# Performance work log

Hardware: AMD Instinct MI355X
Metric: run time of the kernel (lower is better)

The kernel has to match this reference:

```python
import jax, jax.numpy as jnp
import numpy as np

Q_SHAPE = 256      # query block length (default query_shape=(256,))
FLANGE = 256       # memory flange (default memory_flange=(256,))
MAX_REL = 513      # default max_relative_position


def setup_inputs() -> dict:
    key = jax.random.key(0)
    ks = jax.random.split(key, 5)
    B, H, L, D = 2, 8, 8192, 64
    q = jax.random.normal(ks[0], (B, H, L, D), jnp.float32)
    k = jax.random.normal(ks[1], (B, H, L, D), jnp.float32)
    v = jax.random.normal(ks[2], (B, H, L, D), jnp.float32)
    vocab = 2 * MAX_REL + 1
    rel_k_emb = jax.random.normal(ks[3], (vocab, D), jnp.float32) * 0.02
    rel_v_emb = jax.random.normal(ks[4], (vocab, D), jnp.float32) * 0.02
    return {"q": q, "k": k, "v": v, "rel_k_emb": rel_k_emb, "rel_v_emb": rel_v_emb}


def _rel_positions(len_q, len_k, max_rel):
    # generate_relative_positions_matrix: queries aligned to the END of the
    # memory block (range_vec_q = range_vec_k[-len_q:]).
    rk = jnp.arange(len_k)
    rq = rk[-len_q:]
    dist = rk[None, :] - rq[:, None]            # [len_q, len_k]
    return jnp.clip(dist, -max_rel, max_rel) + max_rel


def _masked_local_attention(q, k, v, rel_k_emb, rel_v_emb):
    B, H, L, D = q.shape
    qs, f = Q_SHAPE, FLANGE
    nb = L // qs                                 # number of query blocks
    nf = f // qs
    hp = jax.lax.Precision.HIGHEST

    # fold heads into batch; scale queries.
    qb = (q * (D ** -0.5)).reshape(B * H, nb, qs, D)

    # masked memory blocks: pad LEFT by flange, then memory block i is the
    # concat of blocks [i, ..., i+nf] of the padded sequence -> width qs+f.
    kp = jnp.pad(k.reshape(B * H, L, D), ((0, 0), (f, 0), (0, 0))).reshape(B * H, nb + nf, qs, D)
    vp = jnp.pad(v.reshape(B * H, L, D), ((0, 0), (f, 0), (0, 0))).reshape(B * H, nb + nf, qs, D)
    km = jnp.concatenate([kp[:, s:s + nb] for s in range(nf + 1)], axis=-2)  # [BH, nb, qs+f, D]
    vm = jnp.concatenate([vp[:, s:s + nb] for s in range(nf + 1)], axis=-2)

    mlen = qs + f
    rel = _rel_positions(qs, mlen, MAX_REL)      # [qs, qs+f]
    rk = rel_k_emb[rel]                          # [qs, qs+f, D]
    rv = rel_v_emb[rel]

    # relative_attention_inner (transpose=True): content + position logits.
    logits = (jnp.einsum('bnxd,bnyd->bnxy', qb, km, precision=hp)
              + jnp.einsum('bnxd,xyd->bnxy', qb, rk, precision=hp))

    # causal local mask: global_mem = n*qs - f + mi must satisfy
    # 0 <= global_mem <= global_query = n*qs + qi.
    n = jnp.arange(nb)[:, None, None]
    qi = jnp.arange(qs)[None, :, None]
    mi = jnp.arange(mlen)[None, None, :]
    valid = (mi - f <= qi) & (n * qs + mi >= f)  # [nb, qs, qs+f]
    logits = jnp.where(valid[None], logits, -1e9)

    w = jax.nn.softmax(logits, axis=-1)

    # relative_attention_inner (transpose=False): values + relative values.
    out = (jnp.einsum('bnxy,bnyd->bnxd', w, vm, precision=hp)
           + jnp.einsum('bnxy,xyd->bnxd', w, rv, precision=hp))
    return out.reshape(B, H, L, D)


def reference(q, k, v, rel_k_emb, rel_v_emb):
    return _masked_local_attention(q, k, v, rel_k_emb, rel_v_emb)
```

## Files before the change

kernel.cpp:

```cpp
#include <hip/hip_runtime.h>

typedef __bf16 bf16x8 __attribute__((ext_vector_type(8)));
typedef __bf16 bf16x4 __attribute__((ext_vector_type(4)));
typedef float f32x4 __attribute__((ext_vector_type(4)));

#define LSEQ 8192
#define DDIM 64
#define QS 256
#define CHUNK 128
#define VOCAB 1027
#define RELK_ELEMS (VOCAB * DDIM)
#define RELVT_PITCH 768
#define RELVT_ELEMS (DDIM * RELVT_PITCH)
#define SMAX 10.0f
#define QSCALE 0.18033688011112042f

#define WS_RELK_OFF 0
#define WS_RELVT_OFF 131456
#define WS_KIMG_OFF 229888
#define WS_VIMG_OFF (WS_KIMG_OFF + 16777216)
#define WS_NEED ((size_t)WS_VIMG_OFF + 16777216)

__device__ __forceinline__ int swze(int row) { return ((row ^ (row >> 3)) & 7) << 3; }

__device__ __forceinline__ f32x4 mfma16(bf16x8 a, bf16x8 b, f32x4 c) {
  return __builtin_amdgcn_mfma_f32_16x16x32_bf16(a, b, c, 0, 0, 0);
}

__device__ __forceinline__ float fexp2(float x) { return __builtin_exp2f(x); }

__device__ __forceinline__ void gload16(const __bf16* g, __bf16* l) {
  __builtin_amdgcn_global_load_lds(
      (const __attribute__((address_space(1))) void*)g,
      (__attribute__((address_space(3))) void*)l, 16, 0, 0);
}

__device__ __forceinline__ bf16x8 cvt8(float4 a, float4 b, float sc) {
  bf16x8 r;
  r[0] = (__bf16)(a.x * sc); r[1] = (__bf16)(a.y * sc);
  r[2] = (__bf16)(a.z * sc); r[3] = (__bf16)(a.w * sc);
  r[4] = (__bf16)(b.x * sc); r[5] = (__bf16)(b.y * sc);
  r[6] = (__bf16)(b.z * sc); r[7] = (__bf16)(b.w * sc);
  return r;
}

__global__ void prep_rel(const float* __restrict__ rk, const float* __restrict__ rv,
                         __bf16* __restrict__ relk, __bf16* __restrict__ relvT) {
  int i = blockIdx.x * 256 + threadIdx.x;
  if (i < RELK_ELEMS) relk[i] = (__bf16)rk[i];
  if (i < RELVT_ELEMS) {
    int d = i / RELVT_PITCH, j = i - d * RELVT_PITCH;
    relvT[i] = (__bf16)rv[(j + 2) * DDIM + d];
  }
}

__global__ void prep_kimg(const float* __restrict__ k, __bf16* __restrict__ kimg) {
  int i = blockIdx.x * 256 + threadIdx.x;
  int b = i & 1023;
  int bt = i >> 10;
  int y = b >> 3;
  int d0 = ((b & 7) * 8) ^ swze(y);
  const float* src = k + ((size_t)bt * 128 + y) * DDIM + d0;
  float4 a = *(const float4*)src;
  float4 bb = *(const float4*)(src + 4);
  *(bf16x8*)(kimg + (size_t)i * 8) = cvt8(a, bb, 1.0f);
}

__global__ void prep_vimg(const float* __restrict__ v, __bf16* __restrict__ vimg) {
  __shared__ __align__(16) __bf16 t[CHUNK * DDIM];
  const int bt = blockIdx.x;
  const int tid = threadIdx.x;
  const float* vb = v + (size_t)bt * CHUNK * DDIM;
#pragma unroll
  for (int rep = 0; rep < 4; ++rep) {
    int e = (rep * 256 + tid) * 8;
    float4 a = *(const float4*)(vb + e);
    float4 b = *(const float4*)(vb + e + 4);
    *(bf16x8*)&t[e] = cvt8(a, b, 1.0f);
  }
  __syncthreads();
#pragma unroll
  for (int rep = 0; rep < 4; ++rep) {
    int b = rep * 256 + tid;
    int d = b >> 4;
    int y0 = ((b & 15) * 8) ^ swze(d);
    bf16x8 o8;
#pragma unroll
    for (int j = 0; j < 8; ++j) o8[j] = t[(y0 + j) * DDIM + d];
    *(bf16x8*)(vimg + (size_t)bt * 8192 + (size_t)b * 8) = o8;
  }
}

template <bool PRECONV>
__global__ __launch_bounds__(256, 2) void attn_kernel(
    const float* __restrict__ qg, const float* __restrict__ kg, const float* __restrict__ vg,
    const __bf16* __restrict__ relk, const __bf16* __restrict__ relvT,
    const __bf16* __restrict__ kimg, const __bf16* __restrict__ vimg,
    float* __restrict__ outg) {
  __shared__ __align__(16) __bf16 kbuf[CHUNK * DDIM];
  __shared__ __align__(16) __bf16 vbuf[CHUNK * DDIM];
  __shared__ __align__(16) __bf16 pbuf[64 * CHUNK];
  __shared__ __bf16 ring[4][2][16][18];

  const int phys = blockIdx.x;
  const int xcd = phys & 7;
  const int mseq = phys >> 3;
  const int rg = mseq & 3;
  const int gl = mseq >> 2;
  const int pair = xcd * 64 + gl;
  const int bh = pair >> 5;
  const int nblk = pair & 31;

  const int tid = threadIdx.x;
  const int w = tid >> 6;
  const int lane = tid & 63;
  const int c16 = lane & 15;
  const int grp = lane >> 4;

  const int row_base = rg * 64 + 16 * w;
  const int c0w = 194 - row_base;
  const int j0w = 192 - row_base;
  const int prow = 16 * w + c16;

  const int cstart = (nblk == 0) ? 2 : 0;
  const int c_hi = (rg >= 2) ? 4 : 3;

  auto stage_k = [&](int c) {
    if constexpr (PRECONV) {
      const __bf16* base = kimg + (((size_t)bh * 64 + (size_t)(2 * nblk - 2 + c)) << 13);
      const int boff = 256 * w;
#pragma unroll
      for (int rep = 0; rep < 4; ++rep)
        gload16(base + (size_t)(boff + 64 * rep + lane) * 8, &kbuf[(boff + 64 * rep) * 8]);
    } else {
      const int ty = tid >> 3, td = tid & 7, d0 = td * 8;
      const float* kb = kg + ((size_t)bh * LSEQ + (size_t)(2 * nblk - 2 + c) * CHUNK) * DDIM;
#pragma unroll
      for (int rep = 0; rep < 4; ++rep) {
        int yc = ty + rep * 32;
        const float4* sp = (const float4*)(kb + yc * DDIM + d0);
        *(bf16x8*)&kbuf[yc * 64 + (d0 ^ swze(yc))] = cvt8(sp[0], sp[1], 1.0f);
      }
    }
  };
  auto stage_v = [&](int c) {
    if constexpr (PRECONV) {
      const __bf16* base = vimg + (((size_t)bh * 64 + (size_t)(2 * nblk - 2 + c)) << 13);
      const int boff = 256 * w;
#pragma unroll
      for (int rep = 0; rep < 4; ++rep)
        gload16(base + (size_t)(boff + 64 * rep + lane) * 8, &vbuf[(boff + 64 * rep) * 8]);
    } else {
      const int ty = tid >> 3, td = tid & 7, d0 = td * 8;
      const float* vb = vg + ((size_t)bh * LSEQ + (size_t)(2 * nblk - 2 + c) * CHUNK) * DDIM;
#pragma unroll
      for (int rep = 0; rep < 4; ++rep) {
        int yc = ty + rep * 32;
        const float4* sp = (const float4*)(vb + yc * DDIM + d0);
        float ff[8] = {sp[0].x, sp[0].y, sp[0].z, sp[0].w, sp[1].x, sp[1].y, sp[1].z, sp[1].w};
#pragma unroll
        for (int i = 0; i < 8; ++i) {
          int d = d0 + i;
          vbuf[d * CHUNK + (yc ^ swze(d))] = (__bf16)ff[i];
        }
      }
    }
  };

  bf16x8 qa[2];
  {
    const float* qrow = qg + (size_t)(bh * LSEQ + nblk * QS + row_base + c16) * DDIM;
#pragma unroll
    for (int kk = 0; kk < 2; ++kk) {
      const float4* sp = (const float4*)(qrow + kk * 32 + grp * 8);
      qa[kk] = cvt8(sp[0], sp[1], QSCALE);
    }
  }

  f32x4 o[4];
#pragma unroll
  for (int jd = 0; jd < 4; ++jd) o[jd] = f32x4{0.f, 0.f, 0.f, 0.f};
  float lsum = 0.f;

  auto qr_tile = [&](int ju) {
    f32x4 acc = {0.f, 0.f, 0.f, 0.f};
    int t = c0w + 16 * ju + c16;
    const bf16x8* b0 = (const bf16x8*)(relk + t * DDIM + 8 * grp);
    const bf16x8* b1 = (const bf16x8*)(relk + t * DDIM + 32 + 8 * grp);
    acc = mfma16(*b0, qa[0], acc);
    acc = mfma16(*b1, qa[1], acc);
#pragma unroll
    for (int r = 0; r < 4; ++r) ring[w][ju & 1][4 * grp + r][c16] = (__bf16)acc[r];
  };

  stage_k(cstart);
  __syncthreads();

  for (int c = cstart; c < c_hi; ++c) {
    const bool active = (4 * rg + w + 17 - 8 * c) > 0;

    stage_v(c);

    if (active) {
      if (c == cstart) qr_tile(8 * c + 3);
      float ps = 0.f;
#pragma unroll
      for (int jtl = 0; jtl < 8; ++jtl) {
        const int jt = 8 * c + jtl;
        qr_tile(jt + 4);
        f32x4 acc = {-SMAX, -SMAX, -SMAX, -SMAX};
        int krow = 16 * jtl + c16;
        const bf16x8 aK0 = *(const bf16x8*)&kbuf[krow * 64 + ((8 * grp) ^ swze(krow))];
        const bf16x8 aK1 = *(const bf16x8*)&kbuf[krow * 64 + ((32 + 8 * grp) ^ swze(krow))];
        acc = mfma16(aK0, qa[0], acc);
        acc = mfma16(aK1, qa[1], acc);
        bf16x4 pw;
#pragma unroll
        for (int r = 0; r < 4; ++r) {
          int sk = 4 * grp + r + 15 - c16;
          float qrv = (float)ring[w][(jt + 3 + (sk >> 4)) & 1][sk & 15][c16];
          int yv = 16 * jt + 4 * grp + r;
          float arg = (yv <= row_base + c16 + 256) ? (acc[r] + qrv) : -1e9f;
          float pv = fexp2(arg);
          ps += pv;
          pw[r] = (__bf16)pv;
        }
        *(bf16x4*)&pbuf[prow * CHUNK + ((16 * jtl + 4 * grp) ^ swze(prow))] = pw;
      }
      lsum += ps;
    }

    __syncthreads();

    if (c + 1 < c_hi) stage_k(c + 1);

    if (active) {
      __builtin_amdgcn_s_setprio(1);
#pragma unroll
      for (int ks = 0; ks < 4; ++ks) {
        bf16x8 aP = *(const bf16x8*)&pbuf[prow * CHUNK + ((32 * ks + 8 * grp) ^ swze(prow))];
#pragma unroll
        for (int jd = 0; jd < 4; ++jd) {
          int drow = 16 * jd + c16;
          bf16x8 bV = *(const bf16x8*)&vbuf[drow * CHUNK + ((32 * ks + 8 * grp) ^ swze(drow))];
          o[jd] = mfma16(aP, bV, o[jd]);
        }
      }
      __builtin_amdgcn_s_setprio(0);
#pragma unroll
      for (int s2 = 0; s2 < 5; ++s2) {
        bf16x8 aW;
#pragma unroll
        for (int i = 0; i < 8; ++i) {
          int yl = 32 * s2 + 8 * grp + i + c16 - 31;
          __bf16 pv = (__bf16)0.f;
          if (yl >= 0 && yl < CHUNK) pv = pbuf[prow * CHUNK + (yl ^ swze(prow))];
          aW[i] = pv;
        }
        const int u0 = 128 * c + 32 + 32 * s2 + 8 * grp;
#pragma unroll
        for (int jd = 0; jd < 4; ++jd) {
          int d = 16 * jd + c16;
          const bf16x8* bR = (const bf16x8*)(relvT + d * RELVT_PITCH + j0w + u0);
          o[jd] = mfma16(aW, *bR, o[jd]);
        }
      }
    }

    __syncthreads();
  }

  lsum += __shfl_xor(lsum, 16);
  lsum += __shfl_xor(lsum, 32);
  float inv = 1.0f / lsum;
  float* ob = outg + (size_t)(bh * LSEQ + nblk * QS + row_base) * DDIM;
#pragma unroll
  for (int r = 0; r < 4; ++r) {
    float ir = __shfl(inv, 4 * grp + r);
#pragma unroll
    for (int jd = 0; jd < 4; ++jd) {
      ob[(4 * grp + r) * DDIM + 16 * jd + c16] = o[jd][r] * ir;
    }
  }
}

extern "C" void kernel_launch(void* const* d_in, const int* in_sizes, int n_in,
                              void* d_out, int out_size, void* d_ws, size_t ws_size,
                              hipStream_t stream) {
  const float* q = (const float*)d_in[0];
  const float* k = (const float*)d_in[1];
  const float* v = (const float*)d_in[2];
  const float* rk = (const float*)d_in[3];
  const float* rv = (const float*)d_in[4];

  char* ws = (char*)d_ws;
  __bf16* relk = (__bf16*)(ws + WS_RELK_OFF);
  __bf16* relvT = (__bf16*)(ws + WS_RELVT_OFF);
  __bf16* kimg = (__bf16*)(ws + WS_KIMG_OFF);
  __bf16* vimg = (__bf16*)(ws + WS_VIMG_OFF);

  prep_rel<<<257, 256, 0, stream>>>(rk, rv, relk, relvT);
  if (ws_size >= WS_NEED) {
    prep_kimg<<<4096, 256, 0, stream>>>(k, kimg);
    prep_vimg<<<1024, 256, 0, stream>>>(v, vimg);
    attn_kernel<true><<<2048, 256, 0, stream>>>(q, k, v, relk, relvT, kimg, vimg, (float*)d_out);
  } else {
    attn_kernel<false><<<2048, 256, 0, stream>>>(q, k, v, relk, relvT, relk, relk, (float*)d_out);
  }
}
```

Before: 188.5 us.

## Process two 64-row query groups per block to share staged K/V tiles

Each workgroup now handles two query row groups (rows p*64 and p*64+128) instead of one, halving the grid and reusing each staged K and V chunk across both groups. This removes duplicated global-to-LDS staging of K/V chunks across blocks and balances causal work by pairing a light and a heavy row group. In exchange, register pressure doubles for accumulators and Q fragments, LDS use grows for the doubled pbuf and ring, and occupancy may drop at launch bounds of 2 blocks per CU.

Result: slower. 331.3 us (+75.7%).

```diff
diff --git a/kernel.cpp b/kernel.cpp
--- a/kernel.cpp
+++ b/kernel.cpp
@@ -99,14 +99,14 @@
     float* __restrict__ outg) {
   __shared__ __align__(16) __bf16 kbuf[CHUNK * DDIM];
   __shared__ __align__(16) __bf16 vbuf[CHUNK * DDIM];
-  __shared__ __align__(16) __bf16 pbuf[64 * CHUNK];
-  __shared__ __bf16 ring[4][2][16][18];
+  __shared__ __align__(16) __bf16 pbuf[2 * 64 * CHUNK];
+  __shared__ __bf16 ring[2 * 4 * 2 * 16 * 18];
 
   const int phys = blockIdx.x;
   const int xcd = phys & 7;
   const int mseq = phys >> 3;
-  const int rg = mseq & 3;
-  const int gl = mseq >> 2;
+  const int p = mseq & 1;
+  const int gl = mseq >> 1;
   const int pair = xcd * 64 + gl;
   const int bh = pair >> 5;
   const int nblk = pair & 31;
@@ -117,13 +117,21 @@
   const int c16 = lane & 15;
   const int grp = lane >> 4;
 
-  const int row_base = rg * 64 + 16 * w;
-  const int c0w = 194 - row_base;
-  const int j0w = 192 - row_base;
+  const int row_baseA = 64 * p + 16 * w;
+  const int row_baseB = row_baseA + 128;
+  const int c0wA = 194 - row_baseA;
+  const int c0wB = c0wA - 128;
+  const int j0wA = 192 - row_baseA;
+  const int j0wB = j0wA - 128;
   const int prow = 16 * w + c16;
+  const int xA16 = 4 * p + w;
+
+  __bf16* ringA = &ring[(0 * 4 + w) * 576];
+  __bf16* ringB = &ring[(1 * 4 + w) * 576];
+  __bf16* pbufA = &pbuf[0];
+  __bf16* pbufB = &pbuf[64 * CHUNK];
 
   const int cstart = (nblk == 0) ? 2 : 0;
-  const int c_hi = (rg >= 2) ? 4 : 3;
 
   auto stage_k = [&](int c) {
     if constexpr (PRECONV) {
@@ -167,102 +175,128 @@
     }
   };
 
-  bf16x8 qa[2];
+  bf16x8 qaA[2], qaB[2];
   {
-    const float* qrow = qg + (size_t)(bh * LSEQ + nblk * QS + row_base + c16) * DDIM;
+    const float* qrA = qg + (size_t)(bh * LSEQ + nblk * QS + row_baseA + c16) * DDIM;
+    const float* qrB = qg + (size_t)(bh * LSEQ + nblk * QS + row_baseB + c16) * DDIM;
 #pragma unroll
     for (int kk = 0; kk < 2; ++kk) {
-      const float4* sp = (const float4*)(qrow + kk * 32 + grp * 8);
-      qa[kk] = cvt8(sp[0], sp[1], QSCALE);
-    }
-  }
-
-  f32x4 o[4];
-#pragma unroll
-  for (int jd = 0; jd < 4; ++jd) o[jd] = f32x4{0.f, 0.f, 0.f, 0.f};
-  float lsum = 0.f;
-
-  auto qr_tile = [&](int ju) {
+      const float4* sA = (const float4*)(qrA + kk * 32 + grp * 8);
+      const float4* sB = (const float4*)(qrB + kk * 32 + grp * 8);
+      qaA[kk] = cvt8(sA[0], sA[1], QSCALE);
+      qaB[kk] = cvt8(sB[0], sB[1], QSCALE);
+    }
+  }
+
+  f32x4 oA[4], oB[4];
+#pragma unroll
+  for (int jd = 0; jd < 4; ++jd) { oA[jd] = f32x4{0.f,0.f,0.f,0.f}; oB[jd] = f32x4{0.f,0.f,0.f,0.f}; }
+  float lsumA = 0.f, lsumB = 0.f;
+
+  auto qr_tile = [&](int ju, int c0w_, __bf16* ring_, const bf16x8* qa_) {
     f32x4 acc = {0.f, 0.f, 0.f, 0.f};
-    int t = c0w + 16 * ju + c16;
+    int t = c0w_ + 16 * ju + c16;
     const bf16x8* b0 = (const bf16x8*)(relk + t * DDIM + 8 * grp);
     const bf16x8* b1 = (const bf16x8*)(relk + t * DDIM + 32 + 8 * grp);
-    acc = mfma16(*b0, qa[0], acc);
-    acc = mfma16(*b1, qa[1], acc);
-#pragma unroll
-    for (int r = 0; r < 4; ++r) ring[w][ju & 1][4 * grp + r][c16] = (__bf16)acc[r];
+    acc = mfma16(*b0, qa_[0], acc);
+    acc = mfma16(*b1, qa_[1], acc);
+#pragma unroll
+    for (int r = 0; r < 4; ++r) ring_[(ju & 1) * 288 + (4 * grp + r) * 18 + c16] = (__bf16)acc[r];
+  };
+
+  auto gstep = [&](int jt, bf16x8 aK0, bf16x8 aK1, int c0w_, int row_base_,
+                   __bf16* ring_, __bf16* pbuf_, const bf16x8* qa_, int jtl) -> float {
+    qr_tile(jt + 4, c0w_, ring_, qa_);
+    f32x4 acc = {-SMAX, -SMAX, -SMAX, -SMAX};
+    acc = mfma16(aK0, qa_[0], acc);
+    acc = mfma16(aK1, qa_[1], acc);
+    bf16x4 pw;
+    float ps = 0.f;
+#pragma unroll
+    for (int r = 0; r < 4; ++r) {
+      int sk = 4 * grp + r + 15 - c16;
+      float qrv = (float)ring_[(((jt + 3 + (sk >> 4)) & 1)) * 288 + (sk & 15) * 18 + c16];
+      int yv = 16 * jt + 4 * grp + r;
+      float arg = (yv <= row_base_ + c16 + 256) ? (acc[r] + qrv) : -1e9f;
+      float pv = fexp2(arg);
+      ps += pv;
+      pw[r] = (__bf16)pv;
+    }
+    *(bf16x4*)&pbuf_[prow * CHUNK + ((16 * jtl + 4 * grp) ^ swze(prow))] = pw;
+    return ps;
   };
 
   stage_k(cstart);
   __syncthreads();
 
-  for (int c = cstart; c < c_hi; ++c) {
-    const bool active = (4 * rg + w + 17 - 8 * c) > 0;
+  for (int c = cstart; c < 4; ++c) {
+    const bool activeA = (xA16 + 17 - 8 * c) > 0;
 
     stage_v(c);
 
-    if (active) {
-      if (c == cstart) qr_tile(8 * c + 3);
-      float ps = 0.f;
+    {
+      if (c == cstart) {
+        if (activeA) qr_tile(8 * c + 3, c0wA, ringA, qaA);
+        qr_tile(8 * c + 3, c0wB, ringB, qaB);
+      }
+      float psA = 0.f, psB = 0.f;
 #pragma unroll
       for (int jtl = 0; jtl < 8; ++jtl) {
         const int jt = 8 * c + jtl;
-        qr_tile(jt + 4);
-        f32x4 acc = {-SMAX, -SMAX, -SMAX, -SMAX};
-        int krow = 16 * jtl + c16;
+        const int krow = 16 * jtl + c16;
         const bf16x8 aK0 = *(const bf16x8*)&kbuf[krow * 64 + ((8 * grp) ^ swze(krow))];
         const bf16x8 aK1 = *(const bf16x8*)&kbuf[krow * 64 + ((32 + 8 * grp) ^ swze(krow))];
-        acc = mfma16(aK0, qa[0], acc);
-        acc = mfma16(aK1, qa[1], acc);
-        bf16x4 pw;
-#pragma unroll
-        for (int r = 0; r < 4; ++r) {
-          int sk = 4 * grp + r + 15 - c16;
-          float qrv = (float)ring[w][(jt + 3 + (sk >> 4)) & 1][sk & 15][c16];
-          int yv = 16 * jt + 4 * grp + r;
-          float arg = (yv <= row_base + c16 + 256) ? (acc[r] + qrv) : -1e9f;
-          float pv = fexp2(arg);
-          ps += pv;
-          pw[r] = (__bf16)pv;
+        if (activeA) psA += gstep(jt, aK0, aK1, c0wA, row_baseA, ringA, pbufA, qaA, jtl);
+        psB += gstep(jt, aK0, aK1, c0wB, row_baseB, ringB, pbufB, qaB, jtl);
+      }
+      lsumA += psA;
+      lsumB += psB;
+    }
+
+    __syncthreads();
+
+    if (c + 1 < 4) stage_k(c + 1);
+
+    {
+      __builtin_amdgcn_s_setprio(1);
+#pragma unroll
+      for (int ks = 0; ks < 4; ++ks) {
+        const int po = ((32 * ks + 8 * grp) ^ swze(prow));
+        bf16x8 aPA, aPB;
+        if (activeA) aPA = *(const bf16x8*)&pbufA[prow * CHUNK + po];
+        aPB = *(const bf16x8*)&pbufB[prow * CHUNK + po];
+#pragma unroll
+        for (int jd = 0; jd < 4; ++jd) {
+          const int drow = 16 * jd + c16;
+          const bf16x8 bV = *(const bf16x8*)&vbuf[drow * CHUNK + ((32 * ks + 8 * grp) ^ swze(drow))];
+          if (activeA) oA[jd] = mfma16(aPA, bV, oA[jd]);
+          oB[jd] = mfma16(aPB, bV, oB[jd]);
         }
-        *(bf16x4*)&pbuf[prow * CHUNK + ((16 * jtl + 4 * grp) ^ swze(prow))] = pw;
-      }
-      lsum += ps;
-    }
-
-    __syncthreads();
-
-    if (c + 1 < c_hi) stage_k(c + 1);
-
-    if (active) {
-      __builtin_amdgcn_s_setprio(1);
-#pragma unroll
-      for (int ks = 0; ks < 4; ++ks) {
-        bf16x8 aP = *(const bf16x8*)&pbuf[prow * CHUNK + ((32 * ks + 8 * grp) ^ swze(prow))];
-#pragma unroll
-        for (int jd = 0; jd < 4; ++jd) {
-          int drow = 16 * jd + c16;
-          bf16x8 bV = *(const bf16x8*)&vbuf[drow * CHUNK + ((32 * ks + 8 * grp) ^ swze(drow))];
-          o[jd] = mfma16(aP, bV, o[jd]);
-        }
       }
       __builtin_amdgcn_s_setprio(0);
 #pragma unroll
       for (int s2 = 0; s2 < 5; ++s2) {
-        bf16x8 aW;
+        bf16x8 aWA, aWB;
 #pragma unroll
         for (int i = 0; i < 8; ++i) {
           int yl = 32 * s2 + 8 * grp + i + c16 - 31;
-          __bf16 pv = (__bf16)0.f;
-          if (yl >= 0 && yl < CHUNK) pv = pbuf[prow * CHUNK + (yl ^ swze(prow))];
-          aW[i] = pv;
+          __bf16 pA = (__bf16)0.f, pB = (__bf16)0.f;
+          if (yl >= 0 && yl < CHUNK) {
+            int off = prow * CHUNK + (yl ^ swze(prow));
+            if (activeA) pA = pbufA[off];
+            pB = pbufB[off];
+          }
+          aWA[i] = pA;
+          aWB[i] = pB;
         }
         const int u0 = 128 * c + 32 + 32 * s2 + 8 * grp;
 #pragma unroll
         for (int jd = 0; jd < 4; ++jd) {
-          int d = 16 * jd + c16;
-          const bf16x8* bR = (const bf16x8*)(relvT + d * RELVT_PITCH + j0w + u0);
-          o[jd] = mfma16(aW, *bR, o[jd]);
+          const int d = 16 * jd + c16;
+          const bf16x8* bRA = (const bf16x8*)(relvT + d * RELVT_PITCH + j0wA + u0);
+          const bf16x8* bRB = (const bf16x8*)(relvT + d * RELVT_PITCH + j0wB + u0);
+          if (activeA) oA[jd] = mfma16(aWA, *bRA, oA[jd]);
+          oB[jd] = mfma16(aWB, *bRB, oB[jd]);
         }
       }
     }
@@ -270,16 +304,22 @@
     __syncthreads();
   }
 
-  lsum += __shfl_xor(lsum, 16);
-  lsum += __shfl_xor(lsum, 32);
-  float inv = 1.0f / lsum;
-  float* ob = outg + (size_t)(bh * LSEQ + nblk * QS + row_base) * DDIM;
+  lsumA += __shfl_xor(lsumA, 16);
+  lsumA += __shfl_xor(lsumA, 32);
+  lsumB += __shfl_xor(lsumB, 16);
+  lsumB += __shfl_xor(lsumB, 32);
+  float invA = 1.0f / lsumA;
+  float invB = 1.0f / lsumB;
+  float* obA = outg + (size_t)(bh * LSEQ + nblk * QS + row_baseA) * DDIM;
+  float* obB = outg + (size_t)(bh * LSEQ + nblk * QS + row_baseB) * DDIM;
 #pragma unroll
   for (int r = 0; r < 4; ++r) {
-    float ir = __shfl(inv, 4 * grp + r);
+    float irA = __shfl(invA, 4 * grp + r);
+    float irB = __shfl(invB, 4 * grp + r);
 #pragma unroll
     for (int jd = 0; jd < 4; ++jd) {
-      ob[(4 * grp + r) * DDIM + 16 * jd + c16] = o[jd][r] * ir;
+      obA[(4 * grp + r) * DDIM + 16 * jd + c16] = oA[jd][r] * irA;
+      obB[(4 * grp + r) * DDIM + 16 * jd + c16] = oB[jd][r] * irB;
     }
   }
 }
@@ -303,8 +343,8 @@
   if (ws_size >= WS_NEED) {
     prep_kimg<<<4096, 256, 0, stream>>>(k, kimg);
     prep_vimg<<<1024, 256, 0, stream>>>(v, vimg);
-    attn_kernel<true><<<2048, 256, 0, stream>>>(q, k, v, relk, relvT, kimg, vimg, (float*)d_out);
+    attn_kernel<true><<<1024, 256, 0, stream>>>(q, k, v, relk, relvT, kimg, vimg, (float*)d_out);
   } else {
-    attn_kernel<false><<<2048, 256, 0, stream>>>(q, k, v, relk, relvT, relk, relk, (float*)d_out);
-  }
-}
+    attn_kernel<false><<<1024, 256, 0, stream>>>(q, k, v, relk, relvT, relk, relk, (float*)d_out);
+  }
+}
```
